# Kernel optimization log

Hardware: AMD Instinct MI355X
Metric: run time of the kernel (lower is better)

Reference implementation:

```python
import jax, jax.numpy as jnp
import numpy as np

EMBED_DIM = 1024
HEADS = 16
D_HEAD = EMBED_DIM // HEADS
B, S = 2, 2048


def setup_inputs() -> dict:
    key = jax.random.key(0)
    ks = jax.random.split(key, 7)
    scale = 1.0 / np.sqrt(EMBED_DIM)
    inp = {
        "key": jax.random.normal(ks[0], (B, S, EMBED_DIM), dtype=jnp.float32),
        "query": jax.random.normal(ks[1], (B, S, EMBED_DIM), dtype=jnp.float32),
        "value": jax.random.normal(ks[2], (B, S, EMBED_DIM), dtype=jnp.float32),
        # causal mask, broadcastable to [B, H, Sq, Sk]
        "mask": jnp.tril(jnp.ones((S, S), dtype=bool))[None, None, :, :],
        # torch nn.Linear weights: [out_features, in_features], applied as x @ W.T
        "Wq": jax.random.normal(ks[3], (EMBED_DIM, EMBED_DIM), dtype=jnp.float32) * scale,
        "Wk": jax.random.normal(ks[4], (EMBED_DIM, EMBED_DIM), dtype=jnp.float32) * scale,
        "Wv": jax.random.normal(ks[5], (EMBED_DIM, EMBED_DIM), dtype=jnp.float32) * scale,
        "Wo": jax.random.normal(ks[6], (EMBED_DIM, EMBED_DIM), dtype=jnp.float32) * scale,
    }
    return inp


def reference(key, query, value, mask, Wq, Wk, Wv, Wo):
    b, sq, _ = query.shape
    sk = key.shape[1]
    # projections (torch Linear: x @ W.T), reshape to [B, H, S, Dh]
    q = (query @ Wq.T).reshape(b, sq, HEADS, D_HEAD).transpose(0, 2, 1, 3)
    k = (key @ Wk.T).reshape(b, sk, HEADS, D_HEAD).transpose(0, 2, 1, 3)
    v = (value @ Wv.T).reshape(b, sk, HEADS, D_HEAD).transpose(0, 2, 1, 3)
    # scaled dot-product scores [B, H, Sq, Sk]
    scores = jnp.einsum("bhqd,bhkd->bhqk", q, k) / jnp.sqrt(jnp.float32(D_HEAD))
    scores = jnp.where(mask, scores, jnp.float32(-1e9))
    attn = jax.nn.softmax(scores, axis=-1)
    # dropout p=0.0 -> identity
    out = jnp.einsum("bhqk,bhkd->bhqd", attn, v)  # [B, H, Sq, Dh]
    out = out.transpose(0, 2, 1, 3).reshape(b, sq, EMBED_DIM)
    return out @ Wo.T
```

## Files before the change

kernel.cpp:

```cpp
#include <hip/hip_runtime.h>
#include <stdint.h>


typedef unsigned short ushort_t;
typedef __attribute__((ext_vector_type(8))) __bf16 bf16x8;
typedef __attribute__((ext_vector_type(4))) float floatx4;

#define EMBED 1024
#define SEQ   2048
#define NH    16
#define DH    64
#define QK_SCALE 0.18033688011112042f

__device__ inline ushort_t f2b(float x) {
  unsigned u = __float_as_uint(x);
  u += 0x7FFFu + ((u >> 16) & 1u);
  return (ushort_t)(u >> 16);
}

__device__ inline unsigned pk2(float a, float b) {
  unsigned ua = __float_as_uint(a) + 0x8000u;
  unsigned ub = __float_as_uint(b) + 0x8000u;
  return __builtin_amdgcn_perm(ub, ua, 0x07060302u);
}

__device__ inline void gl_lds16(const ushort_t* g, ushort_t* l) {
  __builtin_amdgcn_global_load_lds(
      (const __attribute__((address_space(1))) unsigned int*)g,
      (__attribute__((address_space(3))) unsigned int*)l, 16, 0, 0);
}

struct CvtArgs {
  const float* src[16];
  ushort_t*    dst[16];
  float        scale[16];
};

__global__ __launch_bounds__(256) void cvt_kernel(CvtArgs a) {
  const int chunk = blockIdx.x >> 9;
  const int off = ((blockIdx.x & 511) << 11) + (threadIdx.x << 3);
  const float sc = a.scale[chunk];
  const float4* s = (const float4*)(a.src[chunk] + off);
  float4 f0 = s[0], f1 = s[1];
  union { ushort_t u[8]; uint4 v; } o;
  o.u[0] = f2b(f0.x * sc); o.u[1] = f2b(f0.y * sc);
  o.u[2] = f2b(f0.z * sc); o.u[3] = f2b(f0.w * sc);
  o.u[4] = f2b(f1.x * sc); o.u[5] = f2b(f1.y * sc);
  o.u[6] = f2b(f1.z * sc); o.u[7] = f2b(f1.w * sc);
  *(uint4*)(a.dst[chunk] + off) = o.v;
}

__device__ inline void store_sub(char* __restrict__ Cv, const int mode,
                                 const int ldc, const int row, const int col,
                                 const floatx4& acc) {
  if (mode == 0) {
    ushort_t* C = (ushort_t*)Cv;
#pragma unroll
    for (int r = 0; r < 4; ++r)
      C[(size_t)(row + r) * ldc + col] = f2b(acc[r]);
  } else if (mode == 1) {
    float* C = (float*)Cv;
#pragma unroll
    for (int r = 0; r < 4; ++r)
      C[(size_t)(row + r) * ldc + col] = acc[r];
  } else {
    ushort_t* C = (ushort_t*)Cv;
    const int b = row >> 11, s = row & 2047;
    const int h = col >> 6, d = col & 63;
    uint2 pk;
    pk.x = pk2(acc[0], acc[1]);
    pk.y = pk2(acc[2], acc[3]);
    *(uint2*)&C[(size_t)((b * NH + h) * DH + d) * SEQ + s] = pk;
  }
}

__device__ inline void gemm512_core(const ushort_t* __restrict__ A,
                                    const ushort_t* __restrict__ W,
                                    char* __restrict__ Cv, const int mode,
                                    const int ldc, const int m0, const int n0) {
  __shared__ ushort_t As[32 * 512];
  __shared__ ushort_t Bs[16 * 512];
  const int tid  = threadIdx.x;
  const int lane = tid & 63;
  const int wid  = tid >> 6;
  const int lm   = lane & 15;
  const int quad = lane >> 4;
  const int wm   = wid >> 1;
  const int wn   = wid & 1;

  floatx4 zero = {0.f, 0.f, 0.f, 0.f};
  floatx4 acc[4][4];
#pragma unroll
  for (int i = 0; i < 4; ++i)
#pragma unroll
    for (int j = 0; j < 4; ++j) acc[i][j] = zero;

  for (int k0 = 0; k0 < EMBED; k0 += 64) {
    __syncthreads();
#pragma unroll
    for (int u = 0; u < 6; ++u) {
      const int c   = wid * 6 + u;
      const int cb  = c & 31;
      const int sub = cb >> 1;
      const int kc  = (cb & 1) * 32 + quad * 8;
      if (c < 32)
        gl_lds16(A + (size_t)(m0 + sub * 16 + lm) * EMBED + k0 + kc, &As[cb * 512]);
      else
        gl_lds16(W + (size_t)(n0 + sub * 16 + lm) * EMBED + k0 + kc, &Bs[cb * 512]);
    }
    __syncthreads();

#pragma unroll
    for (int ks = 0; ks < 2; ++ks) {
      bf16x8 a[4], b[4];
#pragma unroll
      for (int i = 0; i < 4; ++i)
        a[i] = *(const bf16x8*)&As[((wm * 4 + i) * 2 + ks) * 512 + lane * 8];
#pragma unroll
      for (int j = 0; j < 4; ++j)
        b[j] = *(const bf16x8*)&Bs[((wn * 4 + j) * 2 + ks) * 512 + lane * 8];
#pragma unroll
      for (int i = 0; i < 4; ++i)
#pragma unroll
        for (int j = 0; j < 4; ++j)
          acc[i][j] = __builtin_amdgcn_mfma_f32_16x16x32_bf16(a[i], b[j], acc[i][j], 0, 0, 0);
    }
  }

#pragma unroll
  for (int i = 0; i < 4; ++i) {
    const int row = m0 + wm * 64 + i * 16 + quad * 4;
#pragma unroll
    for (int j = 0; j < 4; ++j)
      store_sub(Cv, mode, ldc, row, n0 + wn * 64 + j * 16 + lm, acc[i][j]);
  }
}

struct QkvArgs {
  const ushort_t* A[3];
  const ushort_t* W[3];
  char*           C[3];
};

__global__ __launch_bounds__(512, 4) void qkv_gemm(QkvArgs q) {
  const int z = blockIdx.z;
  gemm512_core(q.A[z], q.W[z], q.C[z], z == 2 ? 2 : 0, EMBED,
               blockIdx.x * 256, blockIdx.y * 128);
}

__global__ __launch_bounds__(256, 4) void o_gemm(const ushort_t* __restrict__ A,
                                                 const ushort_t* __restrict__ W,
                                                 float* __restrict__ C) {
  __shared__ ushort_t As[16 * 512];
  __shared__ ushort_t Bs[8 * 512];
  const int m0 = blockIdx.x * 128, n0 = blockIdx.y * 64;
  const int tid  = threadIdx.x;
  const int lane = tid & 63;
  const int wid  = tid >> 6;
  const int lm   = lane & 15;
  const int quad = lane >> 4;
  const int wm   = wid >> 1;
  const int wn   = wid & 1;

  floatx4 zero = {0.f, 0.f, 0.f, 0.f};
  floatx4 acc[4][2];
#pragma unroll
  for (int i = 0; i < 4; ++i)
#pragma unroll
    for (int j = 0; j < 2; ++j) acc[i][j] = zero;

  for (int k0 = 0; k0 < EMBED; k0 += 64) {
    __syncthreads();
#pragma unroll
    for (int u = 0; u < 6; ++u) {
      const int c   = wid * 6 + u;
      const int cb  = (c < 16) ? c : (c - 16);
      const int sub = cb >> 1;
      const int kc  = (cb & 1) * 32 + quad * 8;
      if (c < 16)
        gl_lds16(A + (size_t)(m0 + sub * 16 + lm) * EMBED + k0 + kc, &As[cb * 512]);
      else
        gl_lds16(W + (size_t)(n0 + sub * 16 + lm) * EMBED + k0 + kc, &Bs[cb * 512]);
    }
    __syncthreads();

#pragma unroll
    for (int ks = 0; ks < 2; ++ks) {
      bf16x8 a[4], b[2];
#pragma unroll
      for (int i = 0; i < 4; ++i)
        a[i] = *(const bf16x8*)&As[((wm * 4 + i) * 2 + ks) * 512 + lane * 8];
#pragma unroll
      for (int j = 0; j < 2; ++j)
        b[j] = *(const bf16x8*)&Bs[((wn * 2 + j) * 2 + ks) * 512 + lane * 8];
#pragma unroll
      for (int i = 0; i < 4; ++i)
#pragma unroll
        for (int j = 0; j < 2; ++j)
          acc[i][j] = __builtin_amdgcn_mfma_f32_16x16x32_bf16(a[i], b[j], acc[i][j], 0, 0, 0);
    }
  }

#pragma unroll
  for (int i = 0; i < 4; ++i) {
    const int row = m0 + wm * 64 + i * 16 + quad * 4;
#pragma unroll
    for (int j = 0; j < 2; ++j) {
      const int col = n0 + wn * 32 + j * 16 + lm;
#pragma unroll
      for (int r = 0; r < 4; ++r)
        C[(size_t)(row + r) * EMBED + col] = acc[i][j][r];
    }
  }
}

__global__ __launch_bounds__(256, 4) void attn_kernel(const ushort_t* __restrict__ Qp,
                                                      const ushort_t* __restrict__ Kp,
                                                      const ushort_t* __restrict__ VpT,
                                                      ushort_t* __restrict__ Ob) {
  __shared__ ushort_t Qs[8 * 512];
  __shared__ ushort_t Ks[2][8 * 512];
  __shared__ ushort_t VTs[2][8 * 512];
  const int L = blockIdx.x;
  const int s8 = (L >> 5) & 7;
  const int g  = L >> 8;
  const int qb = (g == 0) ? s8
               : (g == 1) ? (15 - s8)
               : (g == 2) ? (16 + s8)
                          : (31 - s8);
  const int bh = L & 31;
  const int h = bh & (NH - 1), b = bh >> 4;
  const int tid = threadIdx.x, lane = tid & 63, wid = tid >> 6;
  const int lm = lane & 15, quad = lane >> 4;
  const size_t qkbase = ((size_t)b * SEQ) * EMBED + h * DH;
  const size_t vtbase = ((size_t)(b * NH + h)) * DH * SEQ;

#pragma unroll
  for (int u = 0; u < 2; ++u) {
    const int c = wid * 2 + u;
    gl_lds16(Qp + qkbase + (size_t)(qb * 64 + (c >> 1) * 16 + lm) * EMBED
                 + (c & 1) * 32 + quad * 8,
             &Qs[c * 512]);
  }
#pragma unroll
  for (int u = 0; u < 4; ++u) {
    const int t = wid * 4 + u;
    const int cb = t & 7, sub = cb >> 1, half = cb & 1;
    if (t < 8)
      gl_lds16(Kp + qkbase + (size_t)(sub * 16 + lm) * EMBED + half * 32 + quad * 8,
               &Ks[0][cb * 512]);
    else
      gl_lds16(VpT + vtbase + (size_t)(sub * 16 + lm) * SEQ + half * 32 + quad * 8,
               &VTs[0][cb * 512]);
  }
  asm volatile("s_waitcnt vmcnt(4)" ::: "memory");
  bf16x8 qf[2];
#pragma unroll
  for (int ks = 0; ks < 2; ++ks)
    qf[ks] = *(const bf16x8*)&Qs[(wid * 2 + ks) * 512 + lane * 8];
  ushort_t* pwb = &Qs[wid * 1024];

  float l_part = 0.f;
  floatx4 zero = {0.f, 0.f, 0.f, 0.f};
  floatx4 o_acc[4];
#pragma unroll
  for (int d = 0; d < 4; ++d) o_acc[d] = zero;

  for (int kt = 0; kt <= qb; ++kt) {
    const int cur = kt & 1;
    asm volatile("s_waitcnt vmcnt(0)" ::: "memory");
    __syncthreads();
    if (kt < qb) {
      const int kn = kt + 1;
#pragma unroll
      for (int u = 0; u < 4; ++u) {
        const int t = wid * 4 + u;
        const int cb = t & 7, sub = cb >> 1, half = cb & 1;
        if (t < 8)
          gl_lds16(Kp + qkbase + (size_t)(kn * 64 + sub * 16 + lm) * EMBED
                       + half * 32 + quad * 8,
                   &Ks[cur ^ 1][cb * 512]);
        else
          gl_lds16(VpT + vtbase + (size_t)(sub * 16 + lm) * SEQ
                       + kn * 64 + half * 32 + quad * 8,
                   &VTs[cur ^ 1][cb * 512]);
      }
    }

    floatx4 s_acc[4];
#pragma unroll
    for (int i = 0; i < 4; ++i) s_acc[i] = zero;
    __builtin_amdgcn_s_setprio(1);
#pragma unroll
    for (int ks = 0; ks < 2; ++ks)
#pragma unroll
      for (int i = 0; i < 4; ++i) {
        bf16x8 kf = *(const bf16x8*)&Ks[cur][(i * 2 + ks) * 512 + lane * 8];
        s_acc[i] = __builtin_amdgcn_mfma_f32_16x16x32_bf16(kf, qf[ks], s_acc[i], 0, 0, 0);
      }
    __builtin_amdgcn_s_setprio(0);

    const bool diag = (kt == qb);
#pragma unroll
    for (int i = 0; i < 4; ++i) {
      const int sH = i >> 1;
      const int quadB = ((i & 1) << 1) | (quad >> 1);
      const int gkk = kt * 64 + i * 16 + quad * 4;
      float p[4];
#pragma unroll
      for (int r = 0; r < 4; ++r) p[r] = __builtin_amdgcn_exp2f(s_acc[i][r]);
      if (diag) {
        const int gq = qb * 64 + wid * 16 + lm;
#pragma unroll
        for (int r = 0; r < 4; ++r)
          if (gkk + r > gq) p[r] = 0.f;
      }
#pragma unroll
      for (int r = 0; r < 4; ++r) l_part += p[r];
      uint2 pk;
      pk.x = pk2(p[0], p[1]);
      pk.y = pk2(p[2], p[3]);
      *(uint2*)&pwb[sH * 512 + (quadB * 16 + lm) * 8 + ((quad & 1) << 2)] = pk;
    }
    asm volatile("s_waitcnt lgkmcnt(0)" ::: "memory");

    __builtin_amdgcn_s_setprio(1);
#pragma unroll
    for (int sH = 0; sH < 2; ++sH) {
      bf16x8 pf = *(const bf16x8*)&pwb[sH * 512 + lane * 8];
#pragma unroll
      for (int d = 0; d < 4; ++d) {
        bf16x8 vf = *(const bf16x8*)&VTs[cur][(d * 2 + sH) * 512 + lane * 8];
        o_acc[d] = __builtin_amdgcn_mfma_f32_16x16x32_bf16(vf, pf, o_acc[d], 0, 0, 0);
      }
    }
    __builtin_amdgcn_s_setprio(0);
  }

  {
    float l = l_part;
    l += __shfl_xor(l, 16, 64);
    l += __shfl_xor(l, 32, 64);
    const float inv_l = 1.0f / l;
    const size_t orow = qkbase + (size_t)(qb * 64 + wid * 16 + lm) * EMBED;
#pragma unroll
    for (int d = 0; d < 4; ++d) {
      uint2 pk;
      pk.x = pk2(o_acc[d][0] * inv_l, o_acc[d][1] * inv_l);
      pk.y = pk2(o_acc[d][2] * inv_l, o_acc[d][3] * inv_l);
      *(uint2*)&Ob[orow + d * 16 + quad * 4] = pk;
    }
  }
}

extern "C" void kernel_launch(void* const* d_in, const int* in_sizes, int n_in,
                              void* d_out, int out_size, void* d_ws, size_t ws_size,
                              hipStream_t stream) {
  const float* key   = (const float*)d_in[0];
  const float* query = (const float*)d_in[1];
  const float* value = (const float*)d_in[2];
  const float* Wq = (const float*)d_in[4];
  const float* Wk = (const float*)d_in[5];
  const float* Wv = (const float*)d_in[6];
  const float* Wo = (const float*)d_in[7];

  char* ws = (char*)d_ws;
  const size_t MB = 1024 * 1024;
  ushort_t* Xk  = (ushort_t*)(ws + 0 * MB);
  ushort_t* Xq  = (ushort_t*)(ws + 8 * MB);
  ushort_t* Xv  = (ushort_t*)(ws + 16 * MB);
  ushort_t* Wqb = (ushort_t*)(ws + 24 * MB);
  ushort_t* Wkb = (ushort_t*)(ws + 26 * MB);
  ushort_t* Wvb = (ushort_t*)(ws + 28 * MB);
  ushort_t* Wob = (ushort_t*)(ws + 30 * MB);
  ushort_t* Qp  = (ushort_t*)(ws + 32 * MB);
  ushort_t* Kp  = (ushort_t*)(ws + 40 * MB);
  ushort_t* VpT = (ushort_t*)(ws + 48 * MB);
  ushort_t* Ob  = (ushort_t*)(ws + 56 * MB);

  CvtArgs ca;
  const size_t CE = 1048576;
  for (int c = 0; c < 16; ++c) ca.scale[c] = 1.0f;
  for (int c = 0; c < 4; ++c) { ca.src[c]     = key   + c * CE; ca.dst[c]     = Xk + c * CE; }
  for (int c = 0; c < 4; ++c) { ca.src[4 + c] = query + c * CE; ca.dst[4 + c] = Xq + c * CE; }
  for (int c = 0; c < 4; ++c) { ca.src[8 + c] = value + c * CE; ca.dst[8 + c] = Xv + c * CE; }
  ca.src[12] = Wq; ca.dst[12] = Wqb; ca.scale[12] = QK_SCALE;
  ca.src[13] = Wk; ca.dst[13] = Wkb;
  ca.src[14] = Wv; ca.dst[14] = Wvb;
  ca.src[15] = Wo; ca.dst[15] = Wob;
  cvt_kernel<<<8192, 256, 0, stream>>>(ca);

  QkvArgs qa;
  qa.A[0] = Xq; qa.W[0] = Wqb; qa.C[0] = (char*)Qp;
  qa.A[1] = Xk; qa.W[1] = Wkb; qa.C[1] = (char*)Kp;
  qa.A[2] = Xv; qa.W[2] = Wvb; qa.C[2] = (char*)VpT;
  qkv_gemm<<<dim3(16, 8, 3), 512, 0, stream>>>(qa);

  attn_kernel<<<1024, 256, 0, stream>>>(Qp, Kp, VpT, Ob);

  o_gemm<<<dim3(32, 16), 256, 0, stream>>>(Ob, Wob, (float*)d_out);
}
```

Baseline: 241.8 us.

## Rewrite QKV GEMM as 256x256 double-buffered eight-phase pipelined kernel

Replaces the QKV projection GEMM with a 256x256 tile kernel that double-buffers LDS and splits each K-step into four compute phases. Each phase interleaves a slice of the next tile's global-to-LDS loads with MFMA work, using explicit barriers, vmcnt waits and raised wave priority around the MFMA blocks. Per-block register and LDS use grow (32 accumulators per wave, 128KB LDS), occupancy drops to two blocks, and the grid shrinks to 192 blocks, which may underfill the GPU. Separately, the s_setprio calls in the attention kernel are removed.

Measured after the change: 230.5 us. 4.7% less time.

```diff
diff --git a/kernel.cpp b/kernel.cpp
--- a/kernel.cpp
+++ b/kernel.cpp
@@ -74,65 +74,139 @@
   }
 }
 
-__device__ inline void gemm512_core(const ushort_t* __restrict__ A,
-                                    const ushort_t* __restrict__ W,
-                                    char* __restrict__ Cv, const int mode,
-                                    const int ldc, const int m0, const int n0) {
-  __shared__ ushort_t As[32 * 512];
-  __shared__ ushort_t Bs[16 * 512];
+__device__ inline void stage_pair(const ushort_t* __restrict__ A,
+                                  const ushort_t* __restrict__ W,
+                                  const int m0, const int n0, const int k0,
+                                  ushort_t* __restrict__ Asb,
+                                  ushort_t* __restrict__ Bsb,
+                                  const int wid, const int lm, const int quad,
+                                  const int pair) {
+#pragma unroll
+  for (int e = 0; e < 2; ++e) {
+    const int ul = (pair < 2) ? (pair * 4 + e * 2)
+                              : ((pair - 2) * 4 + e * 2 + 1);
+    const int c  = wid * 8 + ul;
+    const int cb = c & 31;
+    const int sub = cb >> 1;
+    const int kc  = (cb & 1) * 32 + quad * 8;
+    if (c < 32)
+      gl_lds16(A + (size_t)(m0 + sub * 16 + lm) * EMBED + k0 + kc, &Asb[cb * 512]);
+    else
+      gl_lds16(W + (size_t)(n0 + sub * 16 + lm) * EMBED + k0 + kc, &Bsb[cb * 512]);
+  }
+}
+
+__device__ inline void gemm512_8ph(const ushort_t* __restrict__ A,
+                                   const ushort_t* __restrict__ W,
+                                   char* __restrict__ Cv, const int mode,
+                                   const int ldc, const int m0, const int n0) {
+  __shared__ ushort_t As[2][32 * 512];
+  __shared__ ushort_t Bs[2][32 * 512];
   const int tid  = threadIdx.x;
   const int lane = tid & 63;
   const int wid  = tid >> 6;
   const int lm   = lane & 15;
   const int quad = lane >> 4;
-  const int wm   = wid >> 1;
-  const int wn   = wid & 1;
+  const int wm2  = wid >> 2;
+  const int wn4  = wid & 3;
 
   floatx4 zero = {0.f, 0.f, 0.f, 0.f};
-  floatx4 acc[4][4];
-#pragma unroll
-  for (int i = 0; i < 4; ++i)
+  floatx4 acc[8][4];
+#pragma unroll
+  for (int i = 0; i < 8; ++i)
 #pragma unroll
     for (int j = 0; j < 4; ++j) acc[i][j] = zero;
 
-  for (int k0 = 0; k0 < EMBED; k0 += 64) {
-    __syncthreads();
-#pragma unroll
-    for (int u = 0; u < 6; ++u) {
-      const int c   = wid * 6 + u;
-      const int cb  = c & 31;
-      const int sub = cb >> 1;
-      const int kc  = (cb & 1) * 32 + quad * 8;
-      if (c < 32)
-        gl_lds16(A + (size_t)(m0 + sub * 16 + lm) * EMBED + k0 + kc, &As[cb * 512]);
-      else
-        gl_lds16(W + (size_t)(n0 + sub * 16 + lm) * EMBED + k0 + kc, &Bs[cb * 512]);
-    }
-    __syncthreads();
-
-#pragma unroll
-    for (int ks = 0; ks < 2; ++ks) {
-      bf16x8 a[4], b[4];
-#pragma unroll
-      for (int i = 0; i < 4; ++i)
-        a[i] = *(const bf16x8*)&As[((wm * 4 + i) * 2 + ks) * 512 + lane * 8];
+#pragma unroll
+  for (int p = 0; p < 4; ++p)
+    stage_pair(A, W, m0, n0, 0, As[0], Bs[0], wid, lm, quad, p);
+  asm volatile("s_waitcnt vmcnt(4)" ::: "memory");
+  asm volatile("s_barrier" ::: "memory");
+
+#pragma unroll 1
+  for (int t = 0; t < 16; ++t) {
+    const int cur = t & 1;
+    ushort_t* Ac = As[cur];
+    ushort_t* Bc = Bs[cur];
+    ushort_t* An = As[cur ^ 1];
+    ushort_t* Bn = Bs[cur ^ 1];
+    const int kn = (t + 1) << 6;
+    const bool pf = (t < 15);
+
+    bf16x8 a[4], b[4];
+
+#pragma unroll
+    for (int i = 0; i < 4; ++i)
+      a[i] = *(const bf16x8*)&Ac[((wm2 * 8 + i) * 2 + 0) * 512 + lane * 8];
+#pragma unroll
+    for (int j = 0; j < 4; ++j)
+      b[j] = *(const bf16x8*)&Bc[((wn4 * 4 + j) * 2 + 0) * 512 + lane * 8];
+    if (pf) stage_pair(A, W, m0, n0, kn, An, Bn, wid, lm, quad, 0);
+    asm volatile("s_barrier" ::: "memory");
+    __builtin_amdgcn_s_setprio(1);
+#pragma unroll
+    for (int i = 0; i < 4; ++i)
 #pragma unroll
       for (int j = 0; j < 4; ++j)
-        b[j] = *(const bf16x8*)&Bs[((wn * 4 + j) * 2 + ks) * 512 + lane * 8];
-#pragma unroll
-      for (int i = 0; i < 4; ++i)
-#pragma unroll
-        for (int j = 0; j < 4; ++j)
-          acc[i][j] = __builtin_amdgcn_mfma_f32_16x16x32_bf16(a[i], b[j], acc[i][j], 0, 0, 0);
-    }
-  }
-
-#pragma unroll
-  for (int i = 0; i < 4; ++i) {
-    const int row = m0 + wm * 64 + i * 16 + quad * 4;
+        acc[i][j] = __builtin_amdgcn_mfma_f32_16x16x32_bf16(a[i], b[j], acc[i][j], 0, 0, 0);
+    __builtin_amdgcn_s_setprio(0);
+    asm volatile("s_barrier" ::: "memory");
+
+#pragma unroll
+    for (int i = 0; i < 4; ++i)
+      a[i] = *(const bf16x8*)&Ac[((wm2 * 8 + 4 + i) * 2 + 0) * 512 + lane * 8];
+    if (pf) stage_pair(A, W, m0, n0, kn, An, Bn, wid, lm, quad, 1);
+    asm volatile("s_barrier" ::: "memory");
+    __builtin_amdgcn_s_setprio(1);
+#pragma unroll
+    for (int i = 0; i < 4; ++i)
+#pragma unroll
+      for (int j = 0; j < 4; ++j)
+        acc[4 + i][j] = __builtin_amdgcn_mfma_f32_16x16x32_bf16(a[i], b[j], acc[4 + i][j], 0, 0, 0);
+    __builtin_amdgcn_s_setprio(0);
+    if (pf) asm volatile("s_waitcnt vmcnt(4)" ::: "memory");
+    else    asm volatile("s_waitcnt vmcnt(0)" ::: "memory");
+    asm volatile("s_barrier" ::: "memory");
+
+#pragma unroll
+    for (int i = 0; i < 4; ++i)
+      a[i] = *(const bf16x8*)&Ac[((wm2 * 8 + i) * 2 + 1) * 512 + lane * 8];
 #pragma unroll
     for (int j = 0; j < 4; ++j)
-      store_sub(Cv, mode, ldc, row, n0 + wn * 64 + j * 16 + lm, acc[i][j]);
+      b[j] = *(const bf16x8*)&Bc[((wn4 * 4 + j) * 2 + 1) * 512 + lane * 8];
+    if (pf) stage_pair(A, W, m0, n0, kn, An, Bn, wid, lm, quad, 2);
+    asm volatile("s_barrier" ::: "memory");
+    __builtin_amdgcn_s_setprio(1);
+#pragma unroll
+    for (int i = 0; i < 4; ++i)
+#pragma unroll
+      for (int j = 0; j < 4; ++j)
+        acc[i][j] = __builtin_amdgcn_mfma_f32_16x16x32_bf16(a[i], b[j], acc[i][j], 0, 0, 0);
+    __builtin_amdgcn_s_setprio(0);
+    asm volatile("s_barrier" ::: "memory");
+
+#pragma unroll
+    for (int i = 0; i < 4; ++i)
+      a[i] = *(const bf16x8*)&Ac[((wm2 * 8 + 4 + i) * 2 + 1) * 512 + lane * 8];
+    if (pf) stage_pair(A, W, m0, n0, kn, An, Bn, wid, lm, quad, 3);
+    asm volatile("s_barrier" ::: "memory");
+    __builtin_amdgcn_s_setprio(1);
+#pragma unroll
+    for (int i = 0; i < 4; ++i)
+#pragma unroll
+      for (int j = 0; j < 4; ++j)
+        acc[4 + i][j] = __builtin_amdgcn_mfma_f32_16x16x32_bf16(a[i], b[j], acc[4 + i][j], 0, 0, 0);
+    __builtin_amdgcn_s_setprio(0);
+    if (pf) asm volatile("s_waitcnt vmcnt(4)" ::: "memory");
+    asm volatile("s_barrier" ::: "memory");
+  }
+
+#pragma unroll
+  for (int i = 0; i < 8; ++i) {
+    const int row = m0 + wm2 * 128 + i * 16 + quad * 4;
+#pragma unroll
+    for (int j = 0; j < 4; ++j)
+      store_sub(Cv, mode, ldc, row, n0 + wn4 * 64 + j * 16 + lm, acc[i][j]);
   }
 }
 
@@ -142,10 +216,10 @@
   char*           C[3];
 };
 
-__global__ __launch_bounds__(512, 4) void qkv_gemm(QkvArgs q) {
+__global__ __launch_bounds__(512, 2) void qkv_gemm(QkvArgs q) {
   const int z = blockIdx.z;
-  gemm512_core(q.A[z], q.W[z], q.C[z], z == 2 ? 2 : 0, EMBED,
-               blockIdx.x * 256, blockIdx.y * 128);
+  gemm512_8ph(q.A[z], q.W[z], q.C[z], z == 2 ? 2 : 0, EMBED,
+              blockIdx.x * 256, blockIdx.y * 256);
 }
 
 __global__ __launch_bounds__(256, 4) void o_gemm(const ushort_t* __restrict__ A,
@@ -290,7 +364,6 @@
     floatx4 s_acc[4];
 #pragma unroll
     for (int i = 0; i < 4; ++i) s_acc[i] = zero;
-    __builtin_amdgcn_s_setprio(1);
 #pragma unroll
     for (int ks = 0; ks < 2; ++ks)
 #pragma unroll
@@ -298,7 +371,6 @@
         bf16x8 kf = *(const bf16x8*)&Ks[cur][(i * 2 + ks) * 512 + lane * 8];
         s_acc[i] = __builtin_amdgcn_mfma_f32_16x16x32_bf16(kf, qf[ks], s_acc[i], 0, 0, 0);
       }
-    __builtin_amdgcn_s_setprio(0);
 
     const bool diag = (kt == qb);
 #pragma unroll
@@ -324,7 +396,6 @@
     }
     asm volatile("s_waitcnt lgkmcnt(0)" ::: "memory");
 
-    __builtin_amdgcn_s_setprio(1);
 #pragma unroll
     for (int sH = 0; sH < 2; ++sH) {
       bf16x8 pf = *(const bf16x8*)&pwb[sH * 512 + lane * 8];
@@ -334,7 +405,6 @@
         o_acc[d] = __builtin_amdgcn_mfma_f32_16x16x32_bf16(vf, pf, o_acc[d], 0, 0, 0);
       }
     }
-    __builtin_amdgcn_s_setprio(0);
   }
 
   {
@@ -394,7 +464,7 @@
   qa.A[0] = Xq; qa.W[0] = Wqb; qa.C[0] = (char*)Qp;
   qa.A[1] = Xk; qa.W[1] = Wkb; qa.C[1] = (char*)Kp;
   qa.A[2] = Xv; qa.W[2] = Wvb; qa.C[2] = (char*)VpT;
-  qkv_gemm<<<dim3(16, 8, 3), 512, 0, stream>>>(qa);
+  qkv_gemm<<<dim3(16, 4, 3), 512, 0, stream>>>(qa);
 
   attn_kernel<<<1024, 256, 0, stream>>>(Qp, Kp, VpT, Ob);
 
```
